# Optimization experiments

Measured on AMD Instinct MI355X. Metric: run time of the kernel, lower is better.

Reference implementation:

```python
import jax, jax.numpy as jnp
import numpy as np

INPUT_SIZE = 5
HIDDEN = 5
OUT = 1


def setup_inputs() -> dict:
    key = jax.random.key(0)
    ks = jax.random.split(key, 10)
    B, T = 8192, 512
    s_ih = 1.0 / np.sqrt(HIDDEN)
    inp = {
        "x": jax.random.normal(ks[0], (B, T, INPUT_SIZE), dtype=jnp.float32),
        # PyTorch LSTM params: gate order i, f, g, o
        "W_ih": jax.random.uniform(ks[1], (4 * HIDDEN, INPUT_SIZE), minval=-s_ih, maxval=s_ih, dtype=jnp.float32),
        "W_hh": jax.random.uniform(ks[2], (4 * HIDDEN, HIDDEN), minval=-s_ih, maxval=s_ih, dtype=jnp.float32),
        "b_ih": jax.random.uniform(ks[3], (4 * HIDDEN,), minval=-s_ih, maxval=s_ih, dtype=jnp.float32),
        "b_hh": jax.random.uniform(ks[4], (4 * HIDDEN,), minval=-s_ih, maxval=s_ih, dtype=jnp.float32),
        "fc1_w": jax.random.uniform(ks[5], (OUT, HIDDEN), minval=-s_ih, maxval=s_ih, dtype=jnp.float32),
        "fc1_b": jax.random.uniform(ks[6], (OUT,), minval=-s_ih, maxval=s_ih, dtype=jnp.float32),
        "fc2_w": jax.random.uniform(ks[7], (OUT, HIDDEN), minval=-s_ih, maxval=s_ih, dtype=jnp.float32),
        "fc2_b": jax.random.uniform(ks[8], (OUT,), minval=-s_ih, maxval=s_ih, dtype=jnp.float32),
    }
    return inp


def _lstm_last_hidden(x, W_ih, W_hh, b_ih, b_hh):
    # Precompute input contribution for all timesteps in one big GEMM:
    # [B, T, 4H]
    gates_x = jnp.einsum("bti,gi->btg", x, W_ih) + (b_ih + b_hh)
    B = x.shape[0]
    h0 = jnp.zeros((B, HIDDEN), dtype=x.dtype)
    c0 = jnp.zeros((B, HIDDEN), dtype=x.dtype)

    def step(carry, gx):
        h, c = carry
        g = gx + h @ W_hh.T  # [B, 4H]
        i = jax.nn.sigmoid(g[:, 0 * HIDDEN:1 * HIDDEN])
        f = jax.nn.sigmoid(g[:, 1 * HIDDEN:2 * HIDDEN])
        gg = jnp.tanh(g[:, 2 * HIDDEN:3 * HIDDEN])
        o = jax.nn.sigmoid(g[:, 3 * HIDDEN:4 * HIDDEN])
        c_new = f * c + i * gg
        h_new = o * jnp.tanh(c_new)
        return (h_new, c_new), None

    (h_last, _), _ = jax.lax.scan(step, (h0, c0), jnp.swapaxes(gates_x, 0, 1))
    return h_last  # [B, H]


def reference(x, W_ih, W_hh, b_ih, b_hh, fc1_w, fc1_b, fc2_w, fc2_b):
    h = _lstm_last_hidden(x, W_ih, W_hh, b_ih, b_hh)  # out[:, -1, :]
    price = h @ fc1_w.T + fc1_b
    volume = h @ fc2_w.T + fc2_b
    return (price, volume)
```

## Files before the change

kernel.cpp:

```cpp
#include <hip/hip_runtime.h>

#define BTOT 8192
#define TT 512

__device__ __forceinline__ float rcp_f(float x) { return __builtin_amdgcn_rcpf(x); }
__device__ __forceinline__ float exp2_f(float x) { return __builtin_amdgcn_exp2f(x); }
__device__ __forceinline__ float bperm(int addr4, float v) {
    return __int_as_float(__builtin_amdgcn_ds_bpermute(addr4, __float_as_int(v)));
}
__device__ __forceinline__ float dpp_rot1(float v) {
    return __int_as_float(__builtin_amdgcn_mov_dpp(__float_as_int(v), 0x39, 0xf, 0xf, false));
}
__device__ __forceinline__ float dpp_rot2(float v) {
    return __int_as_float(__builtin_amdgcn_mov_dpp(__float_as_int(v), 0x4E, 0xf, 0xf, false));
}
__device__ __forceinline__ float dpp_rot3(float v) {
    return __int_as_float(__builtin_amdgcn_mov_dpp(__float_as_int(v), 0x93, 0xf, 0xf, false));
}

#define LOG2E 1.44269504089f

__global__ __launch_bounds__(64) void lstm_kernel(
    const float* __restrict__ x,
    const float* __restrict__ W_ih,
    const float* __restrict__ W_hh,
    const float* __restrict__ b_ih,
    const float* __restrict__ b_hh,
    const float* __restrict__ fc1_w,
    const float* __restrict__ fc1_b,
    const float* __restrict__ fc2_w,
    const float* __restrict__ fc2_b,
    float* __restrict__ out)
{
    const int lane = threadIdx.x;
    const int ll   = (lane < 60) ? lane : 59;
    const int l    = ll % 20;
    const int base = ll - l;
    const int j    = l >> 2;
    const int g    = l & 3;
    const int b_raw = blockIdx.x * 3 + base / 20;
    const bool write_ok = (lane < 60) && (l == 0) && (b_raw < BTOT);
    const int b = (b_raw < BTOT) ? b_raw : (BTOT - 1);

    const float sc   = (g == 2) ? (2.0f * LOG2E) : (-LOG2E);
    const float selA = (g == 2) ? -2.0f :  1.0f;
    const float selB = (g == 2) ?  1.0f :  0.0f;

    const int row = g * 5 + j;
    float wihs[5], whhs[5];
    #pragma unroll
    for (int i = 0; i < 5; ++i) {
        wihs[i] = sc * W_ih[row * 5 + i];
        whhs[i] = sc * W_hh[row * 5 + i];
    }
    const float bias_s = sc * (b_ih[row] + b_hh[row]);

    int a_h[5];
    #pragma unroll
    for (int k = 0; k < 5; ++k) a_h[k] = (base + 4 * k + 1) << 2;

    const float* xb = x + (size_t)b * (TT * 5);

    float hv[5] = {0.f, 0.f, 0.f, 0.f, 0.f};
    float c = 0.f;

    float4 bufA[5], bufB[5];
    #pragma unroll
    for (int i = 0; i < 5; ++i) {
        bufA[i] = *(const float4*)(xb + 0  + 4 * i);
        bufB[i] = *(const float4*)(xb + 20 + 4 * i);
    }

    auto process4 = [&](const float4* buf) {
        float xs[20];
        *(float4*)&xs[0]  = buf[0];
        *(float4*)&xs[4]  = buf[1];
        *(float4*)&xs[8]  = buf[2];
        *(float4*)&xs[12] = buf[3];
        *(float4*)&xs[16] = buf[4];

        float gx[4];
        #pragma unroll
        for (int s = 0; s < 4; ++s) {
            float a = bias_s;
            #pragma unroll
            for (int i = 0; i < 5; ++i) a = fmaf(wihs[i], xs[s * 5 + i], a);
            gx[s] = a;
        }

        #pragma unroll
        for (int s = 0; s < 4; ++s) {
            float acc = gx[s];
            #pragma unroll
            for (int k = 0; k < 5; ++k) acc = fmaf(whhs[k], hv[k], acc);
            const float val = fmaf(selA, rcp_f(1.0f + exp2_f(acc)), selB);
            const float r1 = dpp_rot1(val);
            const float r2 = dpp_rot2(val);
            const float r3 = dpp_rot3(val);
            c = fmaf(val, c, r3 * r1);
            const float ec = exp2_f(c * (2.0f * LOG2E));
            const float tc = fmaf(-2.0f, rcp_f(1.0f + ec), 1.0f);
            const float h  = r2 * tc;
            #pragma unroll
            for (int k = 0; k < 5; ++k) hv[k] = bperm(a_h[k], h);
        }
    };

    for (int t0 = 0; t0 < TT; t0 += 8) {
        process4(bufA);
        {
            const int tld = (t0 + 8 <= TT - 4) ? (t0 + 8) : (TT - 4);
            const float* p = xb + tld * 5;
            #pragma unroll
            for (int i = 0; i < 5; ++i) bufA[i] = *(const float4*)(p + 4 * i);
        }
        process4(bufB);
        {
            const int tld = (t0 + 12 <= TT - 4) ? (t0 + 12) : (TT - 4);
            const float* p = xb + tld * 5;
            #pragma unroll
            for (int i = 0; i < 5; ++i) bufB[i] = *(const float4*)(p + 4 * i);
        }
    }

    if (write_ok) {
        float p = fc1_b[0];
        float v = fc2_b[0];
        #pragma unroll
        for (int k = 0; k < 5; ++k) {
            p = fmaf(fc1_w[k], hv[k], p);
            v = fmaf(fc2_w[k], hv[k], v);
        }
        out[b] = p;
        out[BTOT + b] = v;
    }
}

extern "C" void kernel_launch(void* const* d_in, const int* in_sizes, int n_in,
                              void* d_out, int out_size, void* d_ws, size_t ws_size,
                              hipStream_t stream) {
    const float* x     = (const float*)d_in[0];
    const float* W_ih  = (const float*)d_in[1];
    const float* W_hh  = (const float*)d_in[2];
    const float* b_ih  = (const float*)d_in[3];
    const float* b_hh  = (const float*)d_in[4];
    const float* fc1_w = (const float*)d_in[5];
    const float* fc1_b = (const float*)d_in[6];
    const float* fc2_w = (const float*)d_in[7];
    const float* fc2_b = (const float*)d_in[8];
    float* out = (float*)d_out;

    const int blocks = (BTOT + 2) / 3;
    lstm_kernel<<<blocks, 64, 0, stream>>>(x, W_ih, W_hh, b_ih, b_hh,
                                           fc1_w, fc1_b, fc2_w, fc2_b, out);
}
```

Baseline: 113.4 us.

## Map four lanes per sequence, one per gate, with DPP quad broadcasts

The per-lane work split changes from 20 lanes per batch element (one gate-unit pair each) to 4 lanes per element (one gate type each, covering all 5 hidden units). Cross-lane exchange now uses quad-broadcast DPP moves instead of ds_bpermute and rotations, which takes LDS permute latency off the recurrent critical path and packs 16 sequences per wave instead of 3. In exchange each lane does about five times more FMA and transcendental work per step and holds more registers, and each element's gate and cell math is duplicated across the four lanes of its quad.

```diff
diff --git a/kernel.cpp b/kernel.cpp
--- a/kernel.cpp
+++ b/kernel.cpp
@@ -2,23 +2,22 @@
 
 #define BTOT 8192
 #define TT 512
+#define LOG2E 1.44269504089f
 
 __device__ __forceinline__ float rcp_f(float x) { return __builtin_amdgcn_rcpf(x); }
 __device__ __forceinline__ float exp2_f(float x) { return __builtin_amdgcn_exp2f(x); }
-__device__ __forceinline__ float bperm(int addr4, float v) {
-    return __int_as_float(__builtin_amdgcn_ds_bpermute(addr4, __float_as_int(v)));
+__device__ __forceinline__ float qb0(float v) {
+    return __int_as_float(__builtin_amdgcn_mov_dpp(__float_as_int(v), 0x00, 0xf, 0xf, false));
 }
-__device__ __forceinline__ float dpp_rot1(float v) {
-    return __int_as_float(__builtin_amdgcn_mov_dpp(__float_as_int(v), 0x39, 0xf, 0xf, false));
+__device__ __forceinline__ float qb1(float v) {
+    return __int_as_float(__builtin_amdgcn_mov_dpp(__float_as_int(v), 0x55, 0xf, 0xf, false));
 }
-__device__ __forceinline__ float dpp_rot2(float v) {
-    return __int_as_float(__builtin_amdgcn_mov_dpp(__float_as_int(v), 0x4E, 0xf, 0xf, false));
+__device__ __forceinline__ float qb2(float v) {
+    return __int_as_float(__builtin_amdgcn_mov_dpp(__float_as_int(v), 0xAA, 0xf, 0xf, false));
 }
-__device__ __forceinline__ float dpp_rot3(float v) {
-    return __int_as_float(__builtin_amdgcn_mov_dpp(__float_as_int(v), 0x93, 0xf, 0xf, false));
+__device__ __forceinline__ float qb3(float v) {
+    return __int_as_float(__builtin_amdgcn_mov_dpp(__float_as_int(v), 0xFF, 0xf, 0xf, false));
 }
-
-#define LOG2E 1.44269504089f
 
 __global__ __launch_bounds__(64) void lstm_kernel(
     const float* __restrict__ x,
@@ -33,36 +32,29 @@
     float* __restrict__ out)
 {
     const int lane = threadIdx.x;
-    const int ll   = (lane < 60) ? lane : 59;
-    const int l    = ll % 20;
-    const int base = ll - l;
-    const int j    = l >> 2;
-    const int g    = l & 3;
-    const int b_raw = blockIdx.x * 3 + base / 20;
-    const bool write_ok = (lane < 60) && (l == 0) && (b_raw < BTOT);
-    const int b = (b_raw < BTOT) ? b_raw : (BTOT - 1);
+    const int g    = lane & 3;
+    const int b    = blockIdx.x * 16 + (lane >> 2);
 
     const float sc   = (g == 2) ? (2.0f * LOG2E) : (-LOG2E);
     const float selA = (g == 2) ? -2.0f :  1.0f;
     const float selB = (g == 2) ?  1.0f :  0.0f;
 
-    const int row = g * 5 + j;
-    float wihs[5], whhs[5];
+    float wih[5][5], whh[5][5], bias[5];
     #pragma unroll
-    for (int i = 0; i < 5; ++i) {
-        wihs[i] = sc * W_ih[row * 5 + i];
-        whhs[i] = sc * W_hh[row * 5 + i];
+    for (int j = 0; j < 5; ++j) {
+        const int row = g * 5 + j;
+        #pragma unroll
+        for (int i = 0; i < 5; ++i) {
+            wih[j][i] = sc * W_ih[row * 5 + i];
+            whh[j][i] = sc * W_hh[row * 5 + i];
+        }
+        bias[j] = sc * (b_ih[row] + b_hh[row]);
     }
-    const float bias_s = sc * (b_ih[row] + b_hh[row]);
-
-    int a_h[5];
-    #pragma unroll
-    for (int k = 0; k < 5; ++k) a_h[k] = (base + 4 * k + 1) << 2;
 
     const float* xb = x + (size_t)b * (TT * 5);
 
     float hv[5] = {0.f, 0.f, 0.f, 0.f, 0.f};
-    float c = 0.f;
+    float cv[5] = {0.f, 0.f, 0.f, 0.f, 0.f};
 
     float4 bufA[5], bufB[5];
     #pragma unroll
@@ -79,30 +71,38 @@
         *(float4*)&xs[12] = buf[3];
         *(float4*)&xs[16] = buf[4];
 
-        float gx[4];
+        float gx[4][5];
         #pragma unroll
-        for (int s = 0; s < 4; ++s) {
-            float a = bias_s;
+        for (int s = 0; s < 4; ++s)
             #pragma unroll
-            for (int i = 0; i < 5; ++i) a = fmaf(wihs[i], xs[s * 5 + i], a);
-            gx[s] = a;
-        }
+            for (int j = 0; j < 5; ++j) {
+                float a = bias[j];
+                #pragma unroll
+                for (int i = 0; i < 5; ++i) a = fmaf(wih[j][i], xs[s * 5 + i], a);
+                gx[s][j] = a;
+            }
 
         #pragma unroll
         for (int s = 0; s < 4; ++s) {
-            float acc = gx[s];
+            float val[5];
             #pragma unroll
-            for (int k = 0; k < 5; ++k) acc = fmaf(whhs[k], hv[k], acc);
-            const float val = fmaf(selA, rcp_f(1.0f + exp2_f(acc)), selB);
-            const float r1 = dpp_rot1(val);
-            const float r2 = dpp_rot2(val);
-            const float r3 = dpp_rot3(val);
-            c = fmaf(val, c, r3 * r1);
-            const float ec = exp2_f(c * (2.0f * LOG2E));
-            const float tc = fmaf(-2.0f, rcp_f(1.0f + ec), 1.0f);
-            const float h  = r2 * tc;
+            for (int j = 0; j < 5; ++j) {
+                float acc = gx[s][j];
+                #pragma unroll
+                for (int k = 0; k < 5; ++k) acc = fmaf(whh[j][k], hv[k], acc);
+                val[j] = fmaf(selA, rcp_f(1.0f + exp2_f(acc)), selB);
+            }
             #pragma unroll
-            for (int k = 0; k < 5; ++k) hv[k] = bperm(a_h[k], h);
+            for (int j = 0; j < 5; ++j) {
+                const float iv = qb0(val[j]);
+                const float fv = qb1(val[j]);
+                const float gv = qb2(val[j]);
+                const float ov = qb3(val[j]);
+                cv[j] = fmaf(fv, cv[j], iv * gv);
+                const float ec = exp2_f(cv[j] * (2.0f * LOG2E));
+                const float tc = fmaf(-2.0f, rcp_f(1.0f + ec), 1.0f);
+                hv[j] = ov * tc;
+            }
         }
     };
 
@@ -123,7 +123,7 @@
         }
     }
 
-    if (write_ok) {
+    if (g == 0) {
         float p = fc1_b[0];
         float v = fc2_b[0];
         #pragma unroll
@@ -150,7 +150,7 @@
     const float* fc2_b = (const float*)d_in[8];
     float* out = (float*)d_out;
 
-    const int blocks = (BTOT + 2) / 3;
+    const int blocks = BTOT / 16;
     lstm_kernel<<<blocks, 64, 0, stream>>>(x, W_ih, W_hh, b_ih, b_hh,
                                            fc1_w, fc1_b, fc2_w, fc2_b, out);
 }
```

Result: slower. 163.3 us (+44.0%).
